# Optimization experiments

Hardware: AMD Instinct MI355X
Metric: run time of the kernel (lower is better)

The kernel has to match this reference:

```python
import jax, jax.numpy as jnp
import numpy as np

B, CIN, COUT, T, H, W = 2, 16, 16, 31, 128, 128


def setup_inputs() -> dict:
    key = jax.random.key(0)
    k1, k2 = jax.random.split(key)
    x = jax.random.normal(k1, (B, CIN, T, H, W), dtype=jnp.float32)
    conv_w = jax.random.normal(k2, (6 * COUT, CIN, 3, 3, 3), dtype=jnp.float32) * 0.05
    conv_b = jnp.zeros((6 * COUT,), dtype=jnp.float32)
    return {"x": x, "conv_w": conv_w, "conv_b": conv_b}


def _sru_scan(f, r, wx, xs):
    """Elementwise SRU recurrence along leading (time) axis.
    All args [T, B, C, H, W].  C_0 = 1 - f_0 (per original code);
    C_t = f_t*C_{t-1} + (1-f_t)*wx_t ;  h_t = r_t*C_t + (1-r_t)*x_t.
    """
    C0 = 1.0 - f[0]
    h0 = r[0] * C0 + (1.0 - r[0]) * xs[0]

    def step(C, inp):
        ft, rt, wxt, xt = inp
        C = ft * C + (1.0 - ft) * wxt
        h = rt * C + (1.0 - rt) * xt
        return C, h

    _, hs = jax.lax.scan(step, C0, (f[1:], r[1:], wx[1:], xs[1:]))
    return jnp.concatenate([h0[None], hs], axis=0)  # [T,B,C,H,W]


def reference(x, conv_w, conv_b):
    # Conv3d: NCDHW, k=3, s=1, p=1 -> shape-preserving, 6*COUT output channels
    gates = jax.lax.conv_general_dilated(
        x, conv_w, window_strides=(1, 1, 1), padding=[(1, 1)] * 3,
        dimension_numbers=("NCDHW", "OIDHW", "NCDHW"))
    gates = gates + conv_b[None, :, None, None, None]

    Wx, ft, ft2, rt, rt2, X = jnp.split(gates, 6, axis=1)
    Wx = jnp.tanh(Wx)
    ft = jax.nn.sigmoid(ft)
    ft2 = jax.nn.sigmoid(ft2)
    rt = jax.nn.sigmoid(rt)
    rt2 = jax.nn.sigmoid(rt2)
    X = jnp.tanh(X)  # act == 'tanh'

    # move band axis (dim 2) to the front for scanning: [T,B,C,H,W]
    tfirst = lambda a: jnp.moveaxis(a, 2, 0)
    Wx_t, ft_t, ft2_t, rt_t, rt2_t, X_t = map(tfirst, (Wx, ft, ft2, rt, rt2, X))

    # left-to-right pass (ft, rt)
    htl = _sru_scan(ft_t, rt_t, Wx_t, X_t)
    # right-to-left pass (ft2, rt2): scan on reversed sequences, reverse back
    rev = lambda a: a[::-1]
    htr = rev(_sru_scan(rev(ft2_t), rev(rt2_t), rev(Wx_t), rev(X_t)))

    out = htl + htr  # [T,B,C,H,W]
    return jnp.moveaxis(out, 0, 2)  # [B,C,T,H,W]
```

## Files before the change

kernel.cpp:

```cpp
#include <hip/hip_runtime.h>

#define DEVFN __device__ __forceinline__

typedef __attribute__((ext_vector_type(8))) short short8;
typedef __attribute__((ext_vector_type(4))) float floatx4;
typedef unsigned short u16;
typedef unsigned int u32;

constexpr int B_   = 2;
constexpr int CIN  = 16;
constexpr int COUT = 16;
constexpr int T_   = 31;
constexpr int H_   = 128;
constexpr int W_   = 128;
constexpr int OC   = 6 * COUT;
constexpr int HW   = H_ * W_;
constexpr int KVOL = CIN * 27;
constexpr int KP   = 448;

constexpr int TP = T_ + 2;
constexpr int HP = H_ + 2;
constexpr int WP = W_ + 2;
constexpr int Sh = WP * 16;
constexpr int St = HP * Sh;
constexpr int NPAD  = B_ * TP * HP * WP;
constexpr int NPADX = NPAD + HP * WP;
constexpr int PADBLK = (NPADX + 255) / 256;
constexpr int WBLK   = (OC * KP + 255) / 256;

constexpr int APH = 7 * 6 * 4 * 16 * 8;

constexpr int GSTR = 268;
constexpr int GS   = 16 * GSTR;
constexpr int GLDS = 6 * GS;

DEVFN float sigmoid_(float v) { return 1.f / (1.f + __expf(-v)); }
DEVFN float tanh_(float v)    { return 1.f - 2.f / (__expf(2.f * v) + 1.f); }

DEVFN u16 f2h(float v) {
  _Float16 h = (_Float16)v;
  u16 u; __builtin_memcpy(&u, &h, 2); return u;
}
DEVFN float h2f(u16 u) {
  _Float16 h; __builtin_memcpy(&h, &u, 2); return (float)h;
}

DEVFN constexpr int dOff(int off) {
  const int o = (off < 27) ? off : 26;
  return (o / 9) * St + ((o % 9) / 3) * Sh + (o % 3) * 16;
}

__global__ __launch_bounds__(256) void prep_kernel(const float* __restrict__ x,
                                                   const float* __restrict__ cw,
                                                   u16* __restrict__ xh,
                                                   u16* __restrict__ wr) {
  if (blockIdx.x < PADBLK) {
    const int idx = blockIdx.x * 256 + threadIdx.x;
    if (idx >= NPADX) return;
    int r = idx;
    const int ww = r % WP; r /= WP;
    const int hh = r % HP; r /= HP;
    const int tt = r % TP; const int b = r / TP;
    const bool in_ = (b < B_) & (tt >= 1) & (tt <= T_) & (hh >= 1) &
                     (hh <= H_) & (ww >= 1) & (ww <= W_);
    const int ts = in_ ? tt - 1 : 0, hs = in_ ? hh - 1 : 0,
              ws = in_ ? ww - 1 : 0;
    const int bs = in_ ? b : 0;
    const float* xp = x + ((size_t)bs * CIN * T_ + ts) * HW + hs * W_ + ws;
    u32 ph[8];
#pragma unroll
    for (int ci = 0; ci < 16; ++ci) {
      const float v = in_ ? xp[ci * (T_ * HW)] : 0.f;
      const u16 hu = f2h(v);
      if (ci & 1) ph[ci >> 1] |= ((u32)hu) << 16;
      else        ph[ci >> 1] = hu;
    }
    uint4* dh = (uint4*)(xh + (size_t)idx * 16);
    dh[0] = make_uint4(ph[0], ph[1], ph[2], ph[3]);
    dh[1] = make_uint4(ph[4], ph[5], ph[6], ph[7]);
  } else {
    const int idx = (blockIdx.x - PADBLK) * 256 + threadIdx.x;
    if (idx >= OC * KP) return;
    const int j    = idx & 7;
    const int n    = (idx >> 3) & 15;
    const int quad = (idx >> 7) & 3;
    const int m    = (idx >> 9) % 6;
    const int s    = idx / 3072;
    const int oc   = m * 16 + n;
    const int k    = s * 32 + quad * 8 + j;
    const int off  = k >> 4, ci = k & 15;
    const float v  = (off < 27) ? cw[oc * KVOL + ci * 27 + off] : 0.f;
    wr[idx] = f2h(v);
  }
}

template <int PH>
DEVFN void kphase(const u16* __restrict__ xp0, const u16* __restrict__ xp1,
                  const u16* __restrict__ xp2, const u16* __restrict__ xp3,
                  const u16* As, int n, int quad, int qhalf,
                  floatx4 (&acc)[6][4]) {
#pragma unroll
  for (int sl = 0; sl < 7; ++sl) {
    const int s = PH * 7 + sl;
    const int d = qhalf ? dOff(2 * s + 1) : dOff(2 * s);
    short8 bh[4];
    bh[0] = *(const short8*)(xp0 + d);
    bh[1] = *(const short8*)(xp1 + d);
    bh[2] = *(const short8*)(xp2 + d);
    bh[3] = *(const short8*)(xp3 + d);
#pragma unroll
    for (int m = 0; m < 6; ++m) {
      const short8 a =
          *(const short8*)(As + (sl * 6 + m) * 512 + quad * 128 + n * 8);
#pragma unroll
      for (int j = 0; j < 4; ++j)
        acc[m][j] =
            __builtin_amdgcn_mfma_f32_16x16x32_f16(a, bh[j], acc[m][j], 0, 0, 0);
    }
  }
}

__global__ __launch_bounds__(256, 3) void conv_sru_fused(
    const u16* __restrict__ xh, const u16* __restrict__ wr,
    const float* __restrict__ cb, float* __restrict__ out) {
  const int lane = threadIdx.x & 63, wv = threadIdx.x >> 6;
  const int n = lane & 15, quad = lane >> 4;
  const int qhalf = quad >> 1, cihalf = quad & 1;
  const int th = n >> 3, wloc = n & 7;
  const int wbase = blockIdx.x * 8;
  const int h = blockIdx.y;
  const int b = blockIdx.z;

  __shared__ __align__(16) u16 As[GLDS];

  const u16* xp0;
  const u16* xp1;
  const u16* xp2;
  const u16* xp3;
  {
    const int t0 = wv * 8 + th;
    const size_t pb = ((size_t)((b * TP + t0) * HP + h) * WP + wbase + wloc) * 16 +
                      cihalf * 8;
    xp0 = xh + pb;
    xp1 = xh + pb + (size_t)2 * St;
    xp2 = xh + pb + (size_t)4 * St;
    xp3 = xh + pb + (size_t)6 * St;
  }

  floatx4 acc[6][4];
#pragma unroll
  for (int m = 0; m < 6; ++m)
#pragma unroll
    for (int j = 0; j < 4; ++j) acc[m][j] = (floatx4)(0.f);

  for (int i = threadIdx.x; i < APH / 8; i += 256)
    ((uint4*)As)[i] = ((const uint4*)wr)[i];
  __syncthreads();
  kphase<0>(xp0, xp1, xp2, xp3, As, n, quad, qhalf, acc);

  __syncthreads();
  for (int i = threadIdx.x; i < APH / 8; i += 256)
    ((uint4*)As)[i] = ((const uint4*)(wr + APH))[i];
  __syncthreads();
  kphase<1>(xp0, xp1, xp2, xp3, As, n, quad, qhalf, acc);

  __syncthreads();
#pragma unroll
  for (int m = 0; m < 6; ++m) {
    const bool isTanh = (m == 0) || (m == 5);
#pragma unroll
    for (int rr = 0; rr < 4; ++rr) {
      const int c = quad * 4 + rr;
      const float bias = cb[m * 16 + c];
#pragma unroll
      for (int j = 0; j < 4; ++j) {
        const int t = wv * 8 + j * 2 + th;
        float v = acc[m][j][rr] + bias;
        v = isTanh ? tanh_(v) : sigmoid_(v);
        As[(m * 16 + c) * GSTR + t * 8 + wloc] = f2h(v);
      }
    }
  }
  __syncthreads();

  const int tid  = threadIdx.x;
  const int half = tid >> 7;
  const int ser  = tid & 127;
  const int c = ser >> 3, w = ser & 7;
  const int gb = c * GSTR + w;

  float htl[T_];
  if (half == 0) {
    float C = 0.f;
#pragma unroll
    for (int t = 0; t < T_; ++t) {
      const float wx = h2f(As[0 * GS + gb + t * 8]);
      const float f  = h2f(As[1 * GS + gb + t * 8]);
      const float r  = h2f(As[3 * GS + gb + t * 8]);
      const float xv = h2f(As[5 * GS + gb + t * 8]);
      C = (t == 0) ? (1.f - f) : (f * C + (1.f - f) * wx);
      htl[t] = r * C + (1.f - r) * xv;
    }
  } else {
    float C2 = 0.f;
#pragma unroll
    for (int t = T_ - 1; t >= 0; --t) {
      const float wx = h2f(As[0 * GS + gb + t * 8]);
      const float f2 = h2f(As[2 * GS + gb + t * 8]);
      const float r2 = h2f(As[4 * GS + gb + t * 8]);
      const float xv = h2f(As[5 * GS + gb + t * 8]);
      C2 = (t == T_ - 1) ? (1.f - f2) : (f2 * C2 + (1.f - f2) * wx);
      const float htr = r2 * C2 + (1.f - r2) * xv;
      const u32 bits = __float_as_uint(htr);
      As[2 * GS + gb + t * 8] = (u16)(bits & 0xffffu);
      As[4 * GS + gb + t * 8] = (u16)(bits >> 16);
    }
  }
  __syncthreads();

  if (half == 0) {
    const size_t ob = ((size_t)(b * COUT + c) * T_) * HW + h * W_ + wbase + w;
#pragma unroll
    for (int t = 0; t < T_; ++t) {
      const u32 lo = As[2 * GS + gb + t * 8];
      const u32 hi = As[4 * GS + gb + t * 8];
      const float htr = __uint_as_float(lo | (hi << 16));
      out[ob + (size_t)t * HW] = htl[t] + htr;
    }
  }
}

__global__ __launch_bounds__(256) void sru_scan_kernel(
    const u16* __restrict__ g, float* __restrict__ out) {
  const int idx  = blockIdx.x * 256 + threadIdx.x;
  const int sp   = idx & (HW - 1);
  const int bc   = idx >> 14;
  const int base = bc * (T_ * HW) + sp;
  const int P    = B_ * COUT * T_ * HW;

  const u16* gWx = g + 0 * P + base;
  const u16* gF  = g + 1 * P + base;
  const u16* gF2 = g + 2 * P + base;
  const u16* gR  = g + 3 * P + base;
  const u16* gR2 = g + 4 * P + base;
  const u16* gX  = g + 5 * P + base;

  float wxs[T_], xs[T_], htl[T_];
  float C = 0.f;
#pragma unroll
  for (int t = 0; t < T_; ++t) {
    const float wx = h2f(gWx[t * HW]);
    const float f  = h2f(gF[t * HW]);
    const float r  = h2f(gR[t * HW]);
    const float xv = h2f(gX[t * HW]);
    wxs[t] = wx;
    xs[t]  = xv;
    C = (t == 0) ? (1.f - f) : (f * C + (1.f - f) * wx);
    htl[t] = r * C + (1.f - r) * xv;
  }
  float C2 = 0.f;
#pragma unroll
  for (int t = T_ - 1; t >= 0; --t) {
    const float f2 = h2f(gF2[t * HW]);
    const float r2 = h2f(gR2[t * HW]);
    C2 = (t == T_ - 1) ? (1.f - f2) : (f2 * C2 + (1.f - f2) * wxs[t]);
    const float htr = r2 * C2 + (1.f - r2) * xs[t];
    out[base + t * HW] = htl[t] + htr;
  }
}

__global__ __launch_bounds__(256) void conv_gates_kernel(
    const float* __restrict__ x, const float* __restrict__ cw,
    const float* __restrict__ cb, u16* __restrict__ gates) {
  const int sp = blockIdx.x * 256 + threadIdx.x;
  const int oc = blockIdx.y;
  const int bt = blockIdx.z;
  const int b  = bt / T_;
  const int t  = bt - b * T_;
  const int h  = sp >> 7;
  const int wc = sp & (W_ - 1);

  __shared__ float wsh[KVOL];
  for (int i = threadIdx.x; i < KVOL; i += 256) wsh[i] = cw[oc * KVOL + i];
  __syncthreads();

  float acc = cb[oc];
  const float* xb = x + b * (CIN * T_ * HW);
  for (int ci = 0; ci < CIN; ++ci) {
    const float* xc = xb + ci * (T_ * HW);
#pragma unroll
    for (int kd = 0; kd < 3; ++kd) {
      const int tt = t + kd - 1;
      if ((unsigned)tt >= (unsigned)T_) continue;
      const float* xt = xc + tt * HW;
#pragma unroll
      for (int kh = 0; kh < 3; ++kh) {
        const int hh = h + kh - 1;
        if ((unsigned)hh >= (unsigned)H_) continue;
        const float* xr = xt + hh * W_;
        const float* wrp = &wsh[(ci * 3 + kd) * 9 + kh * 3];
        if (wc > 0)      acc += wrp[0] * xr[wc - 1];
        acc += wrp[1] * xr[wc];
        if (wc < W_ - 1) acc += wrp[2] * xr[wc + 1];
      }
    }
  }
  const int g = oc >> 4, c = oc & 15;
  const float av = (g == 0 || g == 5) ? tanh_(acc) : sigmoid_(acc);
  const int off = (((g * B_ + b) * COUT + c) * T_ + t) * HW + sp;
  gates[off] = f2h(av);
}

extern "C" void kernel_launch(void* const* d_in, const int* in_sizes, int n_in,
                              void* d_out, int out_size, void* d_ws,
                              size_t ws_size, hipStream_t stream) {
  (void)in_sizes; (void)n_in; (void)out_size;
  const float* x  = (const float*)d_in[0];
  const float* cw = (const float*)d_in[1];
  const float* cb = (const float*)d_in[2];
  float* out = (float*)d_out;

  const size_t planeElems = (size_t)B_ * COUT * T_ * HW;
  const size_t szGatesH = 6 * planeElems * sizeof(u16);
  const size_t szX      = (size_t)NPADX * 16 * sizeof(u16);
  const size_t szW      = (size_t)OC * KP * sizeof(u16);

  char* p = (char*)d_ws;
  if (ws_size >= szX + szW) {
    u16* xh  = (u16*)p;
    u16* wrp = (u16*)(p + szX);
    prep_kernel<<<PADBLK + WBLK, 256, 0, stream>>>(x, cw, xh, wrp);
    const dim3 gfused(W_ / 8, H_, B_);
    conv_sru_fused<<<gfused, 256, 0, stream>>>(xh, wrp, cb, out);
  } else if (ws_size >= szGatesH) {
    u16* gates = (u16*)p;
    const dim3 gdir(HW / 256, OC, B_ * T_);
    conv_gates_kernel<<<gdir, 256, 0, stream>>>(x, cw, cb, gates);
    const int scanBlocks = (B_ * COUT * HW) / 256;
    sru_scan_kernel<<<scanBlocks, 256, 0, stream>>>(gates, out);
  }
}
```

Measured before the change: 269.8 us.

## Stage input tile in LDS via global_load_lds and split output writes

The padded fp16 input window for each block is now loaded once into LDS with async global_load_lds, and the MFMA B operands are read from LDS rather than issued as repeated global loads per kernel offset. The forward scan also stores its hidden states in LDS, so the htl register array goes away and both halves of the block share the final summed store. LDS usage grows and launch bounds drop from 3 to 2 blocks per CU, which cuts occupancy.

Result: slower. 276.6 us (+2.5%).

```diff
diff --git a/kernel.cpp b/kernel.cpp
--- a/kernel.cpp
+++ b/kernel.cpp
@@ -6,6 +6,9 @@
 typedef __attribute__((ext_vector_type(4))) float floatx4;
 typedef unsigned short u16;
 typedef unsigned int u32;
+
+typedef __attribute__((address_space(1))) const void gas_void;
+typedef __attribute__((address_space(3))) void las_void;
 
 constexpr int B_   = 2;
 constexpr int CIN  = 16;
@@ -30,6 +33,11 @@
 
 constexpr int APH = 7 * 6 * 4 * 16 * 8;
 
+constexpr int XCHUNK = 34 * 3 * 20;
+constexpr int XT_OFF = APH;
+constexpr int XT_U16 = 2048 * 8;
+constexpr int LDS_U16 = APH + XT_U16;
+
 constexpr int GSTR = 268;
 constexpr int GS   = 16 * GSTR;
 constexpr int GLDS = 6 * GS;
@@ -43,11 +51,6 @@
 }
 DEVFN float h2f(u16 u) {
   _Float16 h; __builtin_memcpy(&h, &u, 2); return (float)h;
-}
-
-DEVFN constexpr int dOff(int off) {
-  const int o = (off < 27) ? off : 26;
-  return (o / 9) * St + ((o % 9) / 3) * Sh + (o % 3) * 16;
 }
 
 __global__ __launch_bounds__(256) void prep_kernel(const float* __restrict__ x,
@@ -95,19 +98,21 @@
 }
 
 template <int PH>
-DEVFN void kphase(const u16* __restrict__ xp0, const u16* __restrict__ xp1,
-                  const u16* __restrict__ xp2, const u16* __restrict__ xp3,
-                  const u16* As, int n, int quad, int qhalf,
+DEVFN void kphase(const u16* __restrict__ As, const u16* __restrict__ xt,
+                  const int (&bb)[4], int n, int quad, int qhalf,
                   floatx4 (&acc)[6][4]) {
 #pragma unroll
   for (int sl = 0; sl < 7; ++sl) {
-    const int s = PH * 7 + sl;
-    const int d = qhalf ? dOff(2 * s + 1) : dOff(2 * s);
+    const int s  = PH * 7 + sl;
+    const int oE = 2 * s;
+    const int oO = (2 * s + 1 < 27) ? (2 * s + 1) : 26;
+    const int dE = (oE / 9) * 960 + ((oE % 9) / 3) * 320 + (oE % 3) * 32;
+    const int dO = (oO / 9) * 960 + ((oO % 9) / 3) * 320 + (oO % 3) * 32;
+    const int d  = qhalf ? dO : dE;
     short8 bh[4];
-    bh[0] = *(const short8*)(xp0 + d);
-    bh[1] = *(const short8*)(xp1 + d);
-    bh[2] = *(const short8*)(xp2 + d);
-    bh[3] = *(const short8*)(xp3 + d);
+#pragma unroll
+    for (int j = 0; j < 4; ++j)
+      bh[j] = *(const short8*)((const char*)xt + (bb[j] + d));
 #pragma unroll
     for (int m = 0; m < 6; ++m) {
       const short8 a =
@@ -120,7 +125,7 @@
   }
 }
 
-__global__ __launch_bounds__(256, 3) void conv_sru_fused(
+__global__ __launch_bounds__(256, 2) void conv_sru_fused(
     const u16* __restrict__ xh, const u16* __restrict__ wr,
     const float* __restrict__ cb, float* __restrict__ out) {
   const int lane = threadIdx.x & 63, wv = threadIdx.x >> 6;
@@ -131,21 +136,32 @@
   const int h = blockIdx.y;
   const int b = blockIdx.z;
 
-  __shared__ __align__(16) u16 As[GLDS];
-
-  const u16* xp0;
-  const u16* xp1;
-  const u16* xp2;
-  const u16* xp3;
+  __shared__ __align__(16) u16 Ls[LDS_U16];
+  u16* As = Ls;
+  u16* xt = Ls + XT_OFF;
+
   {
-    const int t0 = wv * 8 + th;
-    const size_t pb = ((size_t)((b * TP + t0) * HP + h) * WP + wbase + wloc) * 16 +
-                      cihalf * 8;
-    xp0 = xh + pb;
-    xp1 = xh + pb + (size_t)2 * St;
-    xp2 = xh + pb + (size_t)4 * St;
-    xp3 = xh + pb + (size_t)6 * St;
-  }
+    const u16* xgb = xh + ((size_t)(b * TP) * HP + h) * WP * 16 +
+                     (size_t)wbase * 16;
+#pragma unroll
+    for (int it = 0; it < 8; ++it) {
+      const int cl = it * 256 + (int)threadIdx.x;
+      const int c = (cl < XCHUNK) ? cl : (XCHUNK - 1);
+      const int strip = c / 20;
+      const int o16 = c - strip * 20;
+      const int tt = strip / 3;
+      const int hh = strip - tt * 3;
+      const u16* src = xgb + (size_t)tt * St + hh * Sh + o16 * 8;
+      __builtin_amdgcn_global_load_lds((gas_void*)src,
+                                       (las_void*)(xt + (size_t)cl * 8), 16, 0,
+                                       0);
+    }
+  }
+
+  int bb[4];
+#pragma unroll
+  for (int j = 0; j < 4; ++j)
+    bb[j] = (wv * 8 + j * 2 + th) * 960 + wloc * 32 + cihalf * 16;
 
   floatx4 acc[6][4];
 #pragma unroll
@@ -156,13 +172,13 @@
   for (int i = threadIdx.x; i < APH / 8; i += 256)
     ((uint4*)As)[i] = ((const uint4*)wr)[i];
   __syncthreads();
-  kphase<0>(xp0, xp1, xp2, xp3, As, n, quad, qhalf, acc);
+  kphase<0>(As, xt, bb, n, quad, qhalf, acc);
 
   __syncthreads();
   for (int i = threadIdx.x; i < APH / 8; i += 256)
     ((uint4*)As)[i] = ((const uint4*)(wr + APH))[i];
   __syncthreads();
-  kphase<1>(xp0, xp1, xp2, xp3, As, n, quad, qhalf, acc);
+  kphase<1>(As, xt, bb, n, quad, qhalf, acc);
 
   __syncthreads();
 #pragma unroll
@@ -177,7 +193,7 @@
         const int t = wv * 8 + j * 2 + th;
         float v = acc[m][j][rr] + bias;
         v = isTanh ? tanh_(v) : sigmoid_(v);
-        As[(m * 16 + c) * GSTR + t * 8 + wloc] = f2h(v);
+        Ls[(m * 16 + c) * GSTR + t * 8 + wloc] = f2h(v);
       }
     }
   }
@@ -189,43 +205,48 @@
   const int c = ser >> 3, w = ser & 7;
   const int gb = c * GSTR + w;
 
-  float htl[T_];
   if (half == 0) {
     float C = 0.f;
 #pragma unroll
     for (int t = 0; t < T_; ++t) {
-      const float wx = h2f(As[0 * GS + gb + t * 8]);
-      const float f  = h2f(As[1 * GS + gb + t * 8]);
-      const float r  = h2f(As[3 * GS + gb + t * 8]);
-      const float xv = h2f(As[5 * GS + gb + t * 8]);
+      const float wx = h2f(Ls[0 * GS + gb + t * 8]);
+      const float f  = h2f(Ls[1 * GS + gb + t * 8]);
+      const float r  = h2f(Ls[3 * GS + gb + t * 8]);
+      const float xv = h2f(Ls[5 * GS + gb + t * 8]);
       C = (t == 0) ? (1.f - f) : (f * C + (1.f - f) * wx);
-      htl[t] = r * C + (1.f - r) * xv;
+      const float htl = r * C + (1.f - r) * xv;
+      const u32 bits = __float_as_uint(htl);
+      Ls[1 * GS + gb + t * 8] = (u16)(bits & 0xffffu);
+      Ls[3 * GS + gb + t * 8] = (u16)(bits >> 16);
     }
   } else {
     float C2 = 0.f;
 #pragma unroll
     for (int t = T_ - 1; t >= 0; --t) {
-      const float wx = h2f(As[0 * GS + gb + t * 8]);
-      const float f2 = h2f(As[2 * GS + gb + t * 8]);
-      const float r2 = h2f(As[4 * GS + gb + t * 8]);
-      const float xv = h2f(As[5 * GS + gb + t * 8]);
+      const float wx = h2f(Ls[0 * GS + gb + t * 8]);
+      const float f2 = h2f(Ls[2 * GS + gb + t * 8]);
+      const float r2 = h2f(Ls[4 * GS + gb + t * 8]);
+      const float xv = h2f(Ls[5 * GS + gb + t * 8]);
       C2 = (t == T_ - 1) ? (1.f - f2) : (f2 * C2 + (1.f - f2) * wx);
       const float htr = r2 * C2 + (1.f - r2) * xv;
       const u32 bits = __float_as_uint(htr);
-      As[2 * GS + gb + t * 8] = (u16)(bits & 0xffffu);
-      As[4 * GS + gb + t * 8] = (u16)(bits >> 16);
-    }
-  }
-  __syncthreads();
-
-  if (half == 0) {
+      Ls[2 * GS + gb + t * 8] = (u16)(bits & 0xffffu);
+      Ls[4 * GS + gb + t * 8] = (u16)(bits >> 16);
+    }
+  }
+  __syncthreads();
+
+  {
+    const int tlo = half ? 16 : 0;
+    const int thi = half ? T_ : 16;
     const size_t ob = ((size_t)(b * COUT + c) * T_) * HW + h * W_ + wbase + w;
-#pragma unroll
-    for (int t = 0; t < T_; ++t) {
-      const u32 lo = As[2 * GS + gb + t * 8];
-      const u32 hi = As[4 * GS + gb + t * 8];
-      const float htr = __uint_as_float(lo | (hi << 16));
-      out[ob + (size_t)t * HW] = htl[t] + htr;
+    for (int t = tlo; t < thi; ++t) {
+      const u32 l1 = Ls[1 * GS + gb + t * 8];
+      const u32 h1 = Ls[3 * GS + gb + t * 8];
+      const u32 l2 = Ls[2 * GS + gb + t * 8];
+      const u32 h2 = Ls[4 * GS + gb + t * 8];
+      out[ob + (size_t)t * HW] =
+          __uint_as_float(l1 | (h1 << 16)) + __uint_as_float(l2 | (h2 << 16));
     }
   }
 }
```
